# Optimization experiments

Measured on AMD Instinct MI355X. Metric: run time of the kernel, lower is better.

Reference implementation:

```python
import jax, jax.numpy as jnp
import numpy as np


def setup_inputs() -> dict:
    key = jax.random.key(0)
    k1, k2, k3 = jax.random.split(key, 3)
    bs, S, d, C = 2, 196, 512, 1006
    imgFeaturemap = jax.random.normal(k1, (bs, S, d), dtype=jnp.float32)
    wordFeatures = jax.random.normal(k2, (C, d), dtype=jnp.float32)
    fc3_w = jax.random.normal(k3, (d, d), dtype=jnp.float32) * 0.02
    fc3_b = jnp.zeros((d,), dtype=jnp.float32)
    return {"imgFeaturemap": imgFeaturemap, "wordFeatures": wordFeatures,
            "fc3_w": fc3_w, "fc3_b": fc3_b}


def reference(imgFeaturemap, wordFeatures, fc3_w, fc3_b):
    # imgFeaturemap: (bs, S, d); wordFeatures: (C, d)
    # Broadcast multiply + tanh: (bs, S, C, d)
    t = jnp.tanh(imgFeaturemap[:, :, None, :] * wordFeatures[None, None, :, :])
    # Per-row Linear (PyTorch Linear: x @ W^T + b)
    feat = jnp.einsum('bscd,ed->bsce', t, fc3_w) + fc3_b
    # Softmax over spatial axis S (axis=1), independently per (class, channel)
    coef = jax.nn.softmax(feat, axis=1)
    # Softmax-weighted spatial pooling per class: (bs, C, d)
    semanticFeature = jnp.einsum('bsd,bscd->bcd', imgFeaturemap, coef)
    return semanticFeature
```

## Files before the change

### kernel.cpp

```cpp
#include <hip/hip_runtime.h>

using half8   = __attribute__((ext_vector_type(8))) _Float16;
using half4   = __attribute__((ext_vector_type(4))) _Float16;
using floatx4 = __attribute__((ext_vector_type(4))) float;

namespace {
constexpr int S = 196, D = 512, C = 1006, Cpad = 1024;
constexpr int CB = 32;
constexpr int EBLK = 256;
constexpr int BK = 64;
constexpr int TPB = 256;
constexpr int SCH = 4;
constexpr int SPC = 49;
constexpr int RS = 64;

constexpr size_t W16_BYTES = (size_t)D * D * 2;
constexpr size_t LA_OFF    = W16_BYTES;
constexpr size_t L_BYTES   = (size_t)2 * Cpad * D * 4;
constexpr size_t SL_BYTES  = (size_t)SCH * 2 * Cpad * D * 4;
constexpr size_t SLICE_NEED = LA_OFF + 2 * SL_BYTES;

__device__ __forceinline__ int sw_off(int row, int seg) {
    return row * RS + ((seg ^ (row & 7)) << 3);
}

__device__ __forceinline__ float fast_tanh(float x) {
    float e = __builtin_amdgcn_exp2f(2.885390082f * x);
    return 1.0f - 2.0f * __builtin_amdgcn_rcpf(e + 1.0f);
}

__global__ void prep_w16(const float* __restrict__ fw, _Float16* __restrict__ W16) {
    int i = (blockIdx.x * blockDim.x + threadIdx.x) * 4;
    floatx4 v = *(const floatx4*)&fw[i];
    half4 h;
    h[0] = (_Float16)v[0]; h[1] = (_Float16)v[1];
    h[2] = (_Float16)v[2]; h[3] = (_Float16)v[3];
    *(half4*)&W16[i] = h;
}

__global__ __launch_bounds__(TPB, 2) void semdec_mfma(
    const float* __restrict__ img, const float* __restrict__ word,
    const _Float16* __restrict__ W16,
    float* __restrict__ lbase, float* __restrict__ abase, int use_slice)
{
    __shared__ _Float16 Wc[EBLK * RS];
    __shared__ _Float16 Tc[2 * CB * RS];
    __shared__ float imgL[2][D];

    const int ct = blockIdx.x;
    const int et = blockIdx.y & 1;
    const int b  = blockIdx.y >> 1;
    const int sc = blockIdx.z;

    const int tid  = threadIdx.x;
    const int lane = tid & 63;
    const int ew   = tid >> 6;
    const int l15  = lane & 15;
    const int quad = lane >> 4;

    const int c0 = ct * CB;
    const int e0 = et * EBLK;

    floatx4 lacc[2][4], aacc[2][4];
    #pragma unroll
    for (int ci = 0; ci < 2; ++ci)
        #pragma unroll
        for (int ej = 0; ej < 4; ++ej) {
            lacc[ci][ej] = (floatx4){0.f, 0.f, 0.f, 0.f};
            aacc[ci][ej] = (floatx4){0.f, 0.f, 0.f, 0.f};
        }

    const float* imgB = img + (size_t)b * S * D;
    const int s_base = sc * SPC;

    for (int pr = 0; pr < 25; ++pr) {
        const int s0 = s_base + pr * 2;
        const bool s1v = (pr < 24);
        const int s1 = s1v ? s0 + 1 : s0;

        __syncthreads();
        imgL[0][tid]       = imgB[(size_t)s0 * D + tid];
        imgL[0][tid + 256] = imgB[(size_t)s0 * D + tid + 256];
        imgL[1][tid]       = imgB[(size_t)s1 * D + tid];
        imgL[1][tid + 256] = imgB[(size_t)s1 * D + tid + 256];

        floatx4 acc[2][2][4];
        #pragma unroll
        for (int si = 0; si < 2; ++si)
            #pragma unroll
            for (int ci = 0; ci < 2; ++ci)
                #pragma unroll
                for (int ej = 0; ej < 4; ++ej)
                    acc[si][ci][ej] = (floatx4){0.f, 0.f, 0.f, 0.f};

        for (int kk = 0; kk < D; kk += BK) {
            __syncthreads();
            #pragma unroll
            for (int it = 0; it < 8; ++it) {
                int sid = it * TPB + tid;
                int row = sid >> 3, seg = sid & 7;
                half8 v = *(const half8*)&W16[(size_t)(e0 + row) * D + kk + seg * 8];
                *(half8*)&Wc[sw_off(row, seg)] = v;
            }
            #pragma unroll
            for (int it = 0; it < 2; ++it) {
                int sid = it * TPB + tid;
                int si = sid >> 8, rem = sid & 255;
                int ci32 = rem >> 3, dseg = rem & 7;
                int cg = c0 + ci32; if (cg > C - 1) cg = C - 1;
                const float* wp = &word[(size_t)cg * D + kk + dseg * 8];
                floatx4 w0 = *(const floatx4*)wp;
                floatx4 w1 = *(const floatx4*)(wp + 4);
                const float* ip = &imgL[si][kk + dseg * 8];
                floatx4 i0 = *(const floatx4*)ip;
                floatx4 i1 = *(const floatx4*)(ip + 4);
                half8 t;
                t[0] = (_Float16)fast_tanh(i0[0] * w0[0]);
                t[1] = (_Float16)fast_tanh(i0[1] * w0[1]);
                t[2] = (_Float16)fast_tanh(i0[2] * w0[2]);
                t[3] = (_Float16)fast_tanh(i0[3] * w0[3]);
                t[4] = (_Float16)fast_tanh(i1[0] * w1[0]);
                t[5] = (_Float16)fast_tanh(i1[1] * w1[1]);
                t[6] = (_Float16)fast_tanh(i1[2] * w1[2]);
                t[7] = (_Float16)fast_tanh(i1[3] * w1[3]);
                *(half8*)&Tc[sw_off(si * CB + ci32, dseg)] = t;
            }
            __syncthreads();
            #pragma unroll
            for (int k2 = 0; k2 < BK; k2 += 32) {
                const int jb = (k2 >> 3) + quad;
                half8 af[2][2], bf[4];
                #pragma unroll
                for (int si = 0; si < 2; ++si)
                    #pragma unroll
                    for (int ci = 0; ci < 2; ++ci)
                        af[si][ci] = *(const half8*)&Tc[sw_off(si * CB + ci * 16 + l15, jb)];
                #pragma unroll
                for (int ej = 0; ej < 4; ++ej)
                    bf[ej] = *(const half8*)&Wc[sw_off(ew * 64 + ej * 16 + l15, jb)];
                #pragma unroll
                for (int si = 0; si < 2; ++si)
                    #pragma unroll
                    for (int ci = 0; ci < 2; ++ci)
                        #pragma unroll
                        for (int ej = 0; ej < 4; ++ej)
                            acc[si][ci][ej] = __builtin_amdgcn_mfma_f32_16x16x32_f16(
                                af[si][ci], bf[ej], acc[si][ci][ej], 0, 0, 0);
            }
        }
        #pragma unroll
        for (int si = 0; si < 2; ++si) {
            if (si == 1 && !s1v) break;
            #pragma unroll
            for (int ej = 0; ej < 4; ++ej) {
                float ie = imgL[si][e0 + ew * 64 + ej * 16 + l15];
                #pragma unroll
                for (int ci = 0; ci < 2; ++ci)
                    #pragma unroll
                    for (int r = 0; r < 4; ++r) {
                        float ev = __expf(acc[si][ci][ej][r]);
                        lacc[ci][ej][r] += ev;
                        aacc[ci][ej][r] += ie * ev;
                    }
            }
        }
    }

    if (use_slice) {
        float* lsl = lbase + (size_t)sc * 2 * Cpad * D;
        float* asl = abase + (size_t)sc * 2 * Cpad * D;
        #pragma unroll
        for (int ci = 0; ci < 2; ++ci)
            #pragma unroll
            for (int r = 0; r < 4; ++r) {
                int cg = c0 + ci * 16 + quad * 4 + r;
                #pragma unroll
                for (int ej = 0; ej < 4; ++ej) {
                    int eg = e0 + ew * 64 + ej * 16 + l15;
                    size_t o = ((size_t)b * Cpad + cg) * D + eg;
                    lsl[o] = lacc[ci][ej][r];
                    asl[o] = aacc[ci][ej][r];
                }
            }
    } else {
        #pragma unroll
        for (int ci = 0; ci < 2; ++ci)
            #pragma unroll
            for (int r = 0; r < 4; ++r) {
                int cg = c0 + ci * 16 + quad * 4 + r;
                #pragma unroll
                for (int ej = 0; ej < 4; ++ej) {
                    int eg = e0 + ew * 64 + ej * 16 + l15;
                    atomicAdd(&lbase[((size_t)b * Cpad + cg) * D + eg], lacc[ci][ej][r]);
                    if (cg < C)
                        atomicAdd(&abase[((size_t)b * C + cg) * D + eg], aacc[ci][ej][r]);
                }
            }
    }
}

__global__ void finalize_k(const float* __restrict__ lbase, const float* __restrict__ abase,
                           float* __restrict__ out, int use_slice) {
    int o = blockIdx.x * blockDim.x + threadIdx.x;
    if (o >= 2 * C * D) return;
    int b = o / (C * D);
    int rem = o - b * (C * D);
    int c = rem >> 9;
    int e = rem & (D - 1);
    size_t p = ((size_t)b * Cpad + c) * D + e;
    if (use_slice) {
        float l = 0.f, a = 0.f;
        #pragma unroll
        for (int scn = 0; scn < SCH; ++scn) {
            l += lbase[(size_t)scn * 2 * Cpad * D + p];
            a += abase[(size_t)scn * 2 * Cpad * D + p];
        }
        out[o] = a / l;
    } else {
        out[o] = out[o] / lbase[p];
    }
}

}

extern "C" void kernel_launch(void* const* d_in, const int* in_sizes, int n_in,
                              void* d_out, int out_size, void* d_ws, size_t ws_size,
                              hipStream_t stream) {
    const float* img  = (const float*)d_in[0];
    const float* word = (const float*)d_in[1];
    const float* fw   = (const float*)d_in[2];
    float* out = (float*)d_out;
    char* ws = (char*)d_ws;

    _Float16* W16 = (_Float16*)ws;
    const int use_slice = (ws_size >= SLICE_NEED) ? 1 : 0;

    hipLaunchKernelGGL(prep_w16, dim3(256), dim3(256), 0, stream, fw, W16);

    float *lbase, *abase;
    if (use_slice) {
        lbase = (float*)(ws + LA_OFF);
        abase = (float*)(ws + LA_OFF + SL_BYTES);
    } else {
        lbase = (float*)(ws + LA_OFF);
        abase = out;
        hipMemsetAsync(lbase, 0, L_BYTES, stream);
        hipMemsetAsync(out, 0, (size_t)2 * C * D * 4, stream);
    }

    hipLaunchKernelGGL(semdec_mfma, dim3(32, 4, SCH), dim3(TPB), 0, stream,
                       img, word, W16, lbase, abase, use_slice);

    hipLaunchKernelGGL(finalize_k, dim3((2 * C * D + 255) / 256), dim3(256), 0, stream,
                       lbase, abase, out, use_slice);
}
```

Before: 387.3 us.

## Retile to 4 spatial rows x 16 classes, direct-to-LDS pre-swizzled W loads

Changes the block tile from 2 spatial rows x 32 classes to 4 spatial rows x 16 classes, so each W tile staged in LDS feeds twice as many spatial positions. The grid becomes 64x4x3 with 3 spatial chunks and occupancy 3. The weight matrix is pre-converted into a swizzled fp16 layout so it can be streamed with global_load_lds straight into shared memory, skipping the register round trip. The tanh scale is folded into the image prescale and exp is rewritten as exp2. This costs more LDS for Tc and imgS and leaves uneven pass counts across spatial chunks.

```diff
diff --git a/kernel.cpp b/kernel.cpp
--- a/kernel.cpp
+++ b/kernel.cpp
@@ -1,51 +1,65 @@
 #include <hip/hip_runtime.h>
 
 using half8   = __attribute__((ext_vector_type(8))) _Float16;
-using half4   = __attribute__((ext_vector_type(4))) _Float16;
 using floatx4 = __attribute__((ext_vector_type(4))) float;
 
 namespace {
 constexpr int S = 196, D = 512, C = 1006, Cpad = 1024;
-constexpr int CB = 32;
+constexpr int CB = 16;
 constexpr int EBLK = 256;
 constexpr int BK = 64;
 constexpr int TPB = 256;
-constexpr int SCH = 4;
-constexpr int SPC = 49;
+constexpr int SCH = 3;
 constexpr int RS = 64;
+constexpr float KTANH = 2.885390082f;
+constexpr float INVK  = 0.34657359028f;
 
 constexpr size_t W16_BYTES = (size_t)D * D * 2;
 constexpr size_t LA_OFF    = W16_BYTES;
-constexpr size_t L_BYTES   = (size_t)2 * Cpad * D * 4;
-constexpr size_t SL_BYTES  = (size_t)SCH * 2 * Cpad * D * 4;
+constexpr size_t SLICE_ELEMS = (size_t)2 * Cpad * D;
+constexpr size_t SL_BYTES  = (size_t)SCH * SLICE_ELEMS * 4;
 constexpr size_t SLICE_NEED = LA_OFF + 2 * SL_BYTES;
+constexpr size_t L_BYTES   = SLICE_ELEMS * 4;
 
 __device__ __forceinline__ int sw_off(int row, int seg) {
     return row * RS + ((seg ^ (row & 7)) << 3);
 }
 
-__device__ __forceinline__ float fast_tanh(float x) {
-    float e = __builtin_amdgcn_exp2f(2.885390082f * x);
-    return 1.0f - 2.0f * __builtin_amdgcn_rcpf(e + 1.0f);
-}
-
-__global__ void prep_w16(const float* __restrict__ fw, _Float16* __restrict__ W16) {
-    int i = (blockIdx.x * blockDim.x + threadIdx.x) * 4;
-    floatx4 v = *(const floatx4*)&fw[i];
-    half4 h;
-    h[0] = (_Float16)v[0]; h[1] = (_Float16)v[1];
-    h[2] = (_Float16)v[2]; h[3] = (_Float16)v[3];
-    *(half4*)&W16[i] = h;
-}
-
-__global__ __launch_bounds__(TPB, 2) void semdec_mfma(
+__device__ __forceinline__ void gload16(const _Float16* g, _Float16* l) {
+    __builtin_amdgcn_global_load_lds(
+        (const __attribute__((address_space(1))) unsigned int*)g,
+        (__attribute__((address_space(3))) unsigned int*)l, 16, 0, 0);
+}
+
+__device__ __forceinline__ _Float16 tanh_ps(float y) {
+    float e = __builtin_amdgcn_exp2f(y);
+    return (_Float16)(1.0f - 2.0f * __builtin_amdgcn_rcpf(e + 1.0f));
+}
+
+__global__ void prep_w16sw(const float* __restrict__ fw, _Float16* __restrict__ W16sw) {
+    int id = blockIdx.x * blockDim.x + threadIdx.x;
+    int kki = id >> 12;
+    int r   = (id >> 3) & 511;
+    int j   = id & 7;
+    const float* src = fw + (size_t)r * D + kki * 64 + j * 8;
+    floatx4 v0 = *(const floatx4*)src;
+    floatx4 v1 = *(const floatx4*)(src + 4);
+    half8 h;
+    h[0] = (_Float16)v0[0]; h[1] = (_Float16)v0[1];
+    h[2] = (_Float16)v0[2]; h[3] = (_Float16)v0[3];
+    h[4] = (_Float16)v1[0]; h[5] = (_Float16)v1[1];
+    h[6] = (_Float16)v1[2]; h[7] = (_Float16)v1[3];
+    *(half8*)&W16sw[((size_t)kki << 15) + r * RS + ((j ^ (r & 7)) << 3)] = h;
+}
+
+__global__ __launch_bounds__(TPB, 3) void semdec_mfma(
     const float* __restrict__ img, const float* __restrict__ word,
-    const _Float16* __restrict__ W16,
+    const _Float16* __restrict__ W16sw,
     float* __restrict__ lbase, float* __restrict__ abase, int use_slice)
 {
-    __shared__ _Float16 Wc[EBLK * RS];
-    __shared__ _Float16 Tc[2 * CB * RS];
-    __shared__ float imgL[2][D];
+    __shared__ __align__(16) _Float16 Wc[EBLK * RS];
+    __shared__ __align__(16) _Float16 Tc[4 * CB * RS];
+    __shared__ __align__(16) float imgS[4][D];
 
     const int ct = blockIdx.x;
     const int et = blockIdx.y & 1;
@@ -61,141 +75,133 @@
     const int c0 = ct * CB;
     const int e0 = et * EBLK;
 
-    floatx4 lacc[2][4], aacc[2][4];
+    floatx4 lacc[4], aacc[4];
     #pragma unroll
-    for (int ci = 0; ci < 2; ++ci)
-        #pragma unroll
-        for (int ej = 0; ej < 4; ++ej) {
-            lacc[ci][ej] = (floatx4){0.f, 0.f, 0.f, 0.f};
-            aacc[ci][ej] = (floatx4){0.f, 0.f, 0.f, 0.f};
-        }
+    for (int ej = 0; ej < 4; ++ej) {
+        lacc[ej] = (floatx4){0.f, 0.f, 0.f, 0.f};
+        aacc[ej] = (floatx4){0.f, 0.f, 0.f, 0.f};
+    }
 
     const float* imgB = img + (size_t)b * S * D;
-    const int s_base = sc * SPC;
-
-    for (int pr = 0; pr < 25; ++pr) {
-        const int s0 = s_base + pr * 2;
-        const bool s1v = (pr < 24);
-        const int s1 = s1v ? s0 + 1 : s0;
+    const int s_base = sc * 66;
+    const int npass = (sc < 2) ? 17 : 16;
+
+    for (int pr = 0; pr < npass; ++pr) {
+        const int s0 = s_base + pr * 4;
+        const int slim = (pr == 16) ? 2 : 4;
 
         __syncthreads();
-        imgL[0][tid]       = imgB[(size_t)s0 * D + tid];
-        imgL[0][tid + 256] = imgB[(size_t)s0 * D + tid + 256];
-        imgL[1][tid]       = imgB[(size_t)s1 * D + tid];
-        imgL[1][tid + 256] = imgB[(size_t)s1 * D + tid + 256];
-
-        floatx4 acc[2][2][4];
-        #pragma unroll
-        for (int si = 0; si < 2; ++si)
-            #pragma unroll
-            for (int ci = 0; ci < 2; ++ci)
-                #pragma unroll
-                for (int ej = 0; ej < 4; ++ej)
-                    acc[si][ci][ej] = (floatx4){0.f, 0.f, 0.f, 0.f};
+        #pragma unroll
+        for (int it = 0; it < 2; ++it) {
+            int sid = it * TPB + tid;
+            int si = sid >> 7, pos = (sid & 127) << 2;
+            floatx4 v = *(const floatx4*)&imgB[(size_t)(s0 + si) * D + pos];
+            floatx4 sv = {v[0] * KTANH, v[1] * KTANH, v[2] * KTANH, v[3] * KTANH};
+            *(floatx4*)&imgS[si][pos] = sv;
+        }
+
+        floatx4 acc[4][4];
+        #pragma unroll
+        for (int si = 0; si < 4; ++si)
+            #pragma unroll
+            for (int ej = 0; ej < 4; ++ej)
+                acc[si][ej] = (floatx4){0.f, 0.f, 0.f, 0.f};
 
         for (int kk = 0; kk < D; kk += BK) {
+            const int kki = kk >> 6;
             __syncthreads();
-            #pragma unroll
-            for (int it = 0; it < 8; ++it) {
-                int sid = it * TPB + tid;
-                int row = sid >> 3, seg = sid & 7;
-                half8 v = *(const half8*)&W16[(size_t)(e0 + row) * D + kk + seg * 8];
-                *(half8*)&Wc[sw_off(row, seg)] = v;
+            {
+                const _Float16* wg = W16sw + ((size_t)kki << 15) + ((size_t)e0 << 6);
+                #pragma unroll
+                for (int it = 0; it < 8; ++it) {
+                    int o = ((ew * 8 + it) << 9) + (lane << 3);
+                    gload16(wg + o, &Wc[o]);
+                }
             }
             #pragma unroll
             for (int it = 0; it < 2; ++it) {
                 int sid = it * TPB + tid;
-                int si = sid >> 8, rem = sid & 255;
-                int ci32 = rem >> 3, dseg = rem & 7;
-                int cg = c0 + ci32; if (cg > C - 1) cg = C - 1;
-                const float* wp = &word[(size_t)cg * D + kk + dseg * 8];
+                int si = sid >> 7, rem = sid & 127;
+                int ci = rem >> 3, seg = rem & 7;
+                int cg = c0 + ci; if (cg > C - 1) cg = C - 1;
+                const float* wp = &word[(size_t)cg * D + kk + seg * 8];
                 floatx4 w0 = *(const floatx4*)wp;
                 floatx4 w1 = *(const floatx4*)(wp + 4);
-                const float* ip = &imgL[si][kk + dseg * 8];
+                const float* ip = &imgS[si][kk + seg * 8];
                 floatx4 i0 = *(const floatx4*)ip;
                 floatx4 i1 = *(const floatx4*)(ip + 4);
                 half8 t;
-                t[0] = (_Float16)fast_tanh(i0[0] * w0[0]);
-                t[1] = (_Float16)fast_tanh(i0[1] * w0[1]);
-                t[2] = (_Float16)fast_tanh(i0[2] * w0[2]);
-                t[3] = (_Float16)fast_tanh(i0[3] * w0[3]);
-                t[4] = (_Float16)fast_tanh(i1[0] * w1[0]);
-                t[5] = (_Float16)fast_tanh(i1[1] * w1[1]);
-                t[6] = (_Float16)fast_tanh(i1[2] * w1[2]);
-                t[7] = (_Float16)fast_tanh(i1[3] * w1[3]);
-                *(half8*)&Tc[sw_off(si * CB + ci32, dseg)] = t;
+                t[0] = tanh_ps(i0[0] * w0[0]);
+                t[1] = tanh_ps(i0[1] * w0[1]);
+                t[2] = tanh_ps(i0[2] * w0[2]);
+                t[3] = tanh_ps(i0[3] * w0[3]);
+                t[4] = tanh_ps(i1[0] * w1[0]);
+                t[5] = tanh_ps(i1[1] * w1[1]);
+                t[6] = tanh_ps(i1[2] * w1[2]);
+                t[7] = tanh_ps(i1[3] * w1[3]);
+                *(half8*)&Tc[sw_off(si * CB + ci, seg)] = t;
             }
             __syncthreads();
             #pragma unroll
-            for (int k2 = 0; k2 < BK; k2 += 32) {
-                const int jb = (k2 >> 3) + quad;
-                half8 af[2][2], bf[4];
-                #pragma unroll
-                for (int si = 0; si < 2; ++si)
-                    #pragma unroll
-                    for (int ci = 0; ci < 2; ++ci)
-                        af[si][ci] = *(const half8*)&Tc[sw_off(si * CB + ci * 16 + l15, jb)];
+            for (int k2 = 0; k2 < 2; ++k2) {
+                const int jb = (k2 << 2) + quad;
+                half8 bf[4], af[4];
                 #pragma unroll
                 for (int ej = 0; ej < 4; ++ej)
                     bf[ej] = *(const half8*)&Wc[sw_off(ew * 64 + ej * 16 + l15, jb)];
                 #pragma unroll
-                for (int si = 0; si < 2; ++si)
+                for (int si = 0; si < 4; ++si)
+                    af[si] = *(const half8*)&Tc[sw_off(si * CB + l15, jb)];
+                #pragma unroll
+                for (int si = 0; si < 4; ++si)
                     #pragma unroll
-                    for (int ci = 0; ci < 2; ++ci)
-                        #pragma unroll
-                        for (int ej = 0; ej < 4; ++ej)
-                            acc[si][ci][ej] = __builtin_amdgcn_mfma_f32_16x16x32_f16(
-                                af[si][ci], bf[ej], acc[si][ci][ej], 0, 0, 0);
-            }
-        }
-        #pragma unroll
-        for (int si = 0; si < 2; ++si) {
-            if (si == 1 && !s1v) break;
+                    for (int ej = 0; ej < 4; ++ej)
+                        acc[si][ej] = __builtin_amdgcn_mfma_f32_16x16x32_f16(
+                            af[si], bf[ej], acc[si][ej], 0, 0, 0);
+            }
+        }
+        #pragma unroll
+        for (int si = 0; si < 4; ++si) {
+            if (si >= slim) break;
             #pragma unroll
             for (int ej = 0; ej < 4; ++ej) {
-                float ie = imgL[si][e0 + ew * 64 + ej * 16 + l15];
-                #pragma unroll
-                for (int ci = 0; ci < 2; ++ci)
-                    #pragma unroll
-                    for (int r = 0; r < 4; ++r) {
-                        float ev = __expf(acc[si][ci][ej][r]);
-                        lacc[ci][ej][r] += ev;
-                        aacc[ci][ej][r] += ie * ev;
-                    }
+                float ie = imgS[si][e0 + ew * 64 + ej * 16 + l15] * INVK;
+                #pragma unroll
+                for (int r = 0; r < 4; ++r) {
+                    float ev = __builtin_amdgcn_exp2f(acc[si][ej][r] * 1.44269504f);
+                    lacc[ej][r] += ev;
+                    aacc[ej][r] += ie * ev;
+                }
             }
         }
     }
 
     if (use_slice) {
-        float* lsl = lbase + (size_t)sc * 2 * Cpad * D;
-        float* asl = abase + (size_t)sc * 2 * Cpad * D;
-        #pragma unroll
-        for (int ci = 0; ci < 2; ++ci)
-            #pragma unroll
-            for (int r = 0; r < 4; ++r) {
-                int cg = c0 + ci * 16 + quad * 4 + r;
-                #pragma unroll
-                for (int ej = 0; ej < 4; ++ej) {
-                    int eg = e0 + ew * 64 + ej * 16 + l15;
-                    size_t o = ((size_t)b * Cpad + cg) * D + eg;
-                    lsl[o] = lacc[ci][ej][r];
-                    asl[o] = aacc[ci][ej][r];
-                }
-            }
+        float* lsl = lbase + (size_t)sc * SLICE_ELEMS;
+        float* asl = abase + (size_t)sc * SLICE_ELEMS;
+        #pragma unroll
+        for (int r = 0; r < 4; ++r) {
+            int cg = c0 + quad * 4 + r;
+            #pragma unroll
+            for (int ej = 0; ej < 4; ++ej) {
+                int eg = e0 + ew * 64 + ej * 16 + l15;
+                size_t o = ((size_t)b * Cpad + cg) * D + eg;
+                lsl[o] = lacc[ej][r];
+                asl[o] = aacc[ej][r];
+            }
+        }
     } else {
         #pragma unroll
-        for (int ci = 0; ci < 2; ++ci)
-            #pragma unroll
-            for (int r = 0; r < 4; ++r) {
-                int cg = c0 + ci * 16 + quad * 4 + r;
-                #pragma unroll
-                for (int ej = 0; ej < 4; ++ej) {
-                    int eg = e0 + ew * 64 + ej * 16 + l15;
-                    atomicAdd(&lbase[((size_t)b * Cpad + cg) * D + eg], lacc[ci][ej][r]);
-                    if (cg < C)
-                        atomicAdd(&abase[((size_t)b * C + cg) * D + eg], aacc[ci][ej][r]);
-                }
-            }
+        for (int r = 0; r < 4; ++r) {
+            int cg = c0 + quad * 4 + r;
+            #pragma unroll
+            for (int ej = 0; ej < 4; ++ej) {
+                int eg = e0 + ew * 64 + ej * 16 + l15;
+                atomicAdd(&lbase[((size_t)b * Cpad + cg) * D + eg], lacc[ej][r]);
+                if (cg < C)
+                    atomicAdd(&abase[((size_t)b * C + cg) * D + eg], aacc[ej][r]);
+            }
+        }
     }
 }
 
@@ -212,8 +218,8 @@
         float l = 0.f, a = 0.f;
         #pragma unroll
         for (int scn = 0; scn < SCH; ++scn) {
-            l += lbase[(size_t)scn * 2 * Cpad * D + p];
-            a += abase[(size_t)scn * 2 * Cpad * D + p];
+            l += lbase[(size_t)scn * SLICE_ELEMS + p];
+            a += abase[(size_t)scn * SLICE_ELEMS + p];
         }
         out[o] = a / l;
     } else {
@@ -232,10 +238,10 @@
     float* out = (float*)d_out;
     char* ws = (char*)d_ws;
 
-    _Float16* W16 = (_Float16*)ws;
+    _Float16* W16sw = (_Float16*)ws;
     const int use_slice = (ws_size >= SLICE_NEED) ? 1 : 0;
 
-    hipLaunchKernelGGL(prep_w16, dim3(256), dim3(256), 0, stream, fw, W16);
+    hipLaunchKernelGGL(prep_w16sw, dim3(128), dim3(256), 0, stream, fw, W16sw);
 
     float *lbase, *abase;
     if (use_slice) {
@@ -248,8 +254,8 @@
         hipMemsetAsync(out, 0, (size_t)2 * C * D * 4, stream);
     }
 
-    hipLaunchKernelGGL(semdec_mfma, dim3(32, 4, SCH), dim3(TPB), 0, stream,
-                       img, word, W16, lbase, abase, use_slice);
+    hipLaunchKernelGGL(semdec_mfma, dim3(64, 4, SCH), dim3(TPB), 0, stream,
+                       img, word, W16sw, lbase, abase, use_slice);
 
     hipLaunchKernelGGL(finalize_k, dim3((2 * C * D + 255) / 256), dim3(256), 0, stream,
                        lbase, abase, out, use_slice);
```

Result: faster. 374.7 us (-3.3%).
